# Kernel optimization log

Hardware: AMD Instinct MI355X
Metric: run time of the kernel (lower is better)

## Reference

```python
import jax, jax.numpy as jnp
import numpy as np

T_DIM, BATCH, D_DATA, H_HID = 128, 512, 512, 512
EPS = 1e-8  # torch cosine_similarity eps


def setup_inputs() -> dict:
    key = jax.random.key(0)
    k1, k2, k3, k4, k5 = jax.random.split(key, 5)
    s = 1.0 / np.sqrt(H_HID)  # torch LSTM default init scale
    return {
        "X_tilde": jax.random.normal(k1, (BATCH, T_DIM, D_DATA), jnp.float32),
        "W_ih": jax.random.normal(k2, (4 * H_HID, D_DATA), jnp.float32) * s,
        "W_hh": jax.random.normal(k3, (4 * H_HID, H_HID), jnp.float32) * s,
        "b_ih": jax.random.normal(k4, (4 * H_HID,), jnp.float32) * s,
        "b_hh": jax.random.normal(k5, (4 * H_HID,), jnp.float32) * s,
    }


def _ta_forward(X_tilde, W_ih, W_hh, b_ih, b_hh):
    B, T, D = X_tilde.shape
    H = W_hh.shape[1]

    def lstm_step(carry, x_t):  # x_t: [B, D]
        h, c = carry
        gates = x_t @ W_ih.T + h @ W_hh.T + (b_ih + b_hh)  # [B, 4H]
        i, f, g, o = jnp.split(gates, 4, axis=-1)  # torch gate order i,f,g,o
        i, f, o = jax.nn.sigmoid(i), jax.nn.sigmoid(f), jax.nn.sigmoid(o)
        g = jnp.tanh(g)
        c = f * c + i * g
        h = o * jnp.tanh(c)
        return (h, c), h

    h0 = jnp.zeros((B, H), X_tilde.dtype)
    c0 = jnp.zeros((B, H), X_tilde.dtype)
    # only the first T-1 inputs are fed to the LSTM (last hidden stored pre-step)
    xs = jnp.swapaxes(X_tilde[:, : T - 1, :], 0, 1)  # [T-1, B, D]
    _, hs = jax.lax.scan(lstm_step, (h0, c0), xs)  # [T-1, B, H]
    hidden_tensor = jnp.concatenate([h0[None], hs], axis=0)  # [T, B, H]

    # cosine similarity of each prior hidden (flattened over batch*H) vs final hidden
    ht_prior = hidden_tensor[:-1].reshape(T - 1, -1)  # [T-1, B*H]
    ht_fin = hidden_tensor[-1].reshape(-1)  # [B*H]
    num = ht_prior @ ht_fin  # [T-1]
    denom = jnp.maximum(jnp.linalg.norm(ht_prior, axis=1), EPS) * \
            jnp.maximum(jnp.linalg.norm(ht_fin), EPS)
    alpha = jax.nn.softmax(num / denom, axis=0)  # [T-1]

    ht_final = jnp.sum(alpha[:, None, None] * hidden_tensor[:-1], axis=0)  # [B, H]
    return ht_final[None]  # [1, B, H]


def reference(X_tilde, W_ih, W_hh, b_ih, b_hh):
    return _ta_forward(X_tilde, W_ih, W_hh, b_ih, b_hh)
```

## Files before the change

kernel.cpp:

```cpp
#include <hip/hip_runtime.h>
#include <stdint.h>

#define T_DIM  128
#define TSTEPS 127
#define BATCH  512
#define DDATA  512
#define HHID   512
#define BH     262144
#define CPAD   132

typedef _Float16 f16;
typedef _Float16 f16x8 __attribute__((ext_vector_type(8)));
typedef float    f32x4 __attribute__((ext_vector_type(4)));
typedef unsigned int u32x2 __attribute__((ext_vector_type(2)));

#define MFMA16 __builtin_amdgcn_mfma_f32_16x16x32_f16

__device__ __forceinline__ f16x8 ld16(const f16* p) {
  f16x8 r;
  asm volatile("global_load_dwordx4 %0, %1, off" : "=v"(r) : "v"(p));
  return r;
}
__device__ __forceinline__ f16x8 ld16cc(const f16* p) {
  f16x8 r;
  asm volatile("global_load_dwordx4 %0, %1, off sc0 sc1" : "=v"(r) : "v"(p));
  return r;
}
__device__ __forceinline__ void st8cc(void* p, u32x2 v) {
  asm volatile("global_store_dwordx2 %0, %1, off sc0 sc1" :: "v"(p), "v"(v) : "memory");
}

#define BAR_LGKM do { asm volatile("s_waitcnt lgkmcnt(0)\n\ts_barrier" ::: "memory"); } while (0)

__global__ void k_prep_w(const float* __restrict__ W_ih, const float* __restrict__ W_hh,
                         f16* __restrict__ W16B) {
  int d = blockIdx.x * blockDim.x + threadIdx.x;
  int lane = d & 63;
  int fi   = (d >> 6) & 31;
  int ch   = (d >> 11) & 1;
  int kq   = (d >> 12) & 3;
  int nbv  = d >> 14;
  int ks = fi >> 2, nf = fi & 3;
  int col16 = lane & 15, lk2 = lane >> 4;
  int hm = col16 >> 2, g = col16 & 3;
  int hg = nbv * 32 + (ch * 4 + nf) * 4 + hm;
  int R = g * 512 + hg;
  int k = kq * 256 + ks * 32 + lk2 * 8;
  const float* src = (k < 512) ? (W_ih + (size_t)R * 512 + k)
                               : (W_hh + (size_t)R * 512 + (k - 512));
  f16x8 o;
#pragma unroll
  for (int e = 0; e < 8; e++) o[e] = (f16)src[e];
  *(f16x8*)(W16B + (size_t)d * 8) = o;
}

__global__ void k_prep_b(const float* __restrict__ b_ih, const float* __restrict__ b_hh,
                         float* __restrict__ biasR) {
  int r = blockIdx.x * blockDim.x + threadIdx.x;
  if (r < 2048) biasR[r] = b_ih[r] + b_hh[r];
}

__global__ void k_prep_x(const float* __restrict__ X, f16* __restrict__ XT) {
  __shared__ f16 Ls[32][516];
  const int t = blockIdx.x;
  const int rb = blockIdx.y;
  const int tid = threadIdx.x;
  const int rloc = tid >> 5;
  const int dc = (tid & 31) * 16;
#pragma unroll
  for (int it = 0; it < 4; it++) {
    int row = it * 8 + rloc;
    const float* src = X + (size_t)(rb * 32 + row) * (T_DIM * DDATA)
                         + (size_t)t * DDATA + dc;
    f32x4 a0 = *(const f32x4*)(src);
    f32x4 a1 = *(const f32x4*)(src + 4);
    f32x4 a2 = *(const f32x4*)(src + 8);
    f32x4 a3 = *(const f32x4*)(src + 12);
    f16x8 h0, h1;
#pragma unroll
    for (int e = 0; e < 4; e++) {
      h0[e] = (f16)a0[e]; h0[4 + e] = (f16)a1[e];
      h1[e] = (f16)a2[e]; h1[4 + e] = (f16)a3[e];
    }
    *(f16x8*)&Ls[row][dc] = h0;
    *(f16x8*)&Ls[row][dc + 8] = h1;
  }
  __syncthreads();
#pragma unroll
  for (int it = 0; it < 8; it++) {
    int chunk = it * 256 + tid;
    int kc = chunk >> 5, row = chunk & 31;
    f16x8 v = *(const f16x8*)&Ls[row][kc * 8];
    *(f16x8*)(XT + (size_t)t * BH + (size_t)kc * 4096
              + (size_t)(rb * 32 + row) * 8) = v;
  }
}

__launch_bounds__(512, 1)
__global__ void k_lstm(const f16* __restrict__ XT, f16* __restrict__ h_all,
                       const f16* __restrict__ W16B, const float* __restrict__ biasR) {
  __shared__ float C[4][32][CPAD];
  __shared__ float BiasS[128];

  const int tid = threadIdx.x, lane = tid & 63, w = tid >> 6;
  const int kq = w >> 1;
  const int wg = blockIdx.x;
  const int mb = (wg & 7) * 2 + ((wg >> 3) & 1);
  const int nb = wg >> 4;
  const int m0 = mb * 32;
  const int l15 = lane & 15, lk = lane >> 4;

  f16x8 B[32];
  {
    const f16* wb = W16B + ((size_t)((nb * 4 + kq) * 2 + (w & 1)) * 32) * 512 + lane * 8;
#pragma unroll
    for (int i = 0; i < 32; i++) B[i] = ld16(wb + i * 512);
    asm volatile("s_waitcnt vmcnt(0)" ::: "memory");
    __builtin_amdgcn_sched_barrier(0);
  }
  if (tid < 128) {
    int q8 = tid >> 4, hm = (tid >> 2) & 3, g = tid & 3;
    BiasS[tid] = biasR[g * 512 + nb * 32 + q8 * 4 + hm];
  }
  float c_reg[4] = {0.f, 0.f, 0.f, 0.f};
  __syncthreads();

#define WAITV(N) asm volatile("s_waitcnt vmcnt(" #N ")" ::: "memory");        \
                 __builtin_amdgcn_sched_barrier(0)
#define MFMA4KS(KS0)                                                          \
    {                                                                         \
      _Pragma("unroll")                                                       \
      for (int s = 0; s < 4; s++) {                                           \
        int ks = KS0 + s;                                                     \
        _Pragma("unroll")                                                     \
        for (int nf = 0; nf < 4; nf++) {                                      \
          acc[0][nf] = MFMA16(R[2 * ks],     B[ks * 4 + nf], acc[0][nf], 0, 0, 0); \
          acc[1][nf] = MFMA16(R[2 * ks + 1], B[ks * 4 + nf], acc[1][nf], 0, 0, 0); \
        }                                                                     \
      }                                                                       \
    }
#define ISSUE_X(T)                                                            \
    {                                                                         \
      const f16* Ab = XT + (size_t)(T) * BH + (size_t)(kq * 32 + lk) * 4096   \
                      + (size_t)(m0 + l15) * 8;                               \
      _Pragma("unroll")                                                       \
      for (int ks = 0; ks < 8; ks++) {                                        \
        R[2 * ks]     = ld16(Ab + (size_t)ks * 16384);                        \
        R[2 * ks + 1] = ld16(Ab + (size_t)ks * 16384 + 128);                  \
      }                                                                       \
    }

  f16x8 R[16];
  if (kq < 2) ISSUE_X(0);

  for (int t = 0; t < TSTEPS; t++) {
    f32x4 acc[2][4] = {};

    if (kq < 2) {
      WAITV(0);
      MFMA4KS(0);
      MFMA4KS(4);
      if (t + 1 < TSTEPS) ISSUE_X(t + 1);
    } else if (t > 0) {
      const f16* Hb = h_all + (size_t)t * BH + (size_t)((kq - 2) * 32 + lk) * 4096
                      + (size_t)(m0 + l15) * 8;
      int rounds = 0;
      while (true) {
#pragma unroll
        for (int ks = 0; ks < 8; ks++) {
          R[2 * ks]     = ld16cc(Hb + (size_t)ks * 16384);
          R[2 * ks + 1] = ld16cc(Hb + (size_t)ks * 16384 + 128);
        }
        WAITV(0);
        unsigned bad = 0;
#pragma unroll
        for (int i = 0; i < 16; i++) {
          const unsigned* u = (const unsigned*)&R[i];
          bad |= (unsigned)(u[0] == 0xFFFFFFFFu) | (unsigned)(u[2] == 0xFFFFFFFFu);
        }
        if (__all(bad == 0)) break;
        if (++rounds > 4096) break;
        __builtin_amdgcn_s_sleep(1);
      }
      MFMA4KS(0);
      MFMA4KS(4);
    }

#pragma unroll
    for (int mf = 0; mf < 2; mf++)
#pragma unroll
      for (int nf = 0; nf < 4; nf++)
#pragma unroll
        for (int r = 0; r < 4; r++)
          C[kq][mf * 16 + lk * 4 + r][(w & 1) * 64 + nf * 16 + l15] = acc[mf][nf][r];
    BAR_LGKM;

    if (tid < 256) {
      int r = tid >> 3, q8 = tid & 7;
      f32x4 uu[4] = {};
#pragma unroll
      for (int q = 0; q < 4; q++) {
        const f32x4* base = (const f32x4*)&C[q][r][q8 * 16];
        uu[0] += base[0];
        uu[1] += base[1];
        uu[2] += base[2];
        uu[3] += base[3];
      }
      union { f16 h[4]; u32x2 v; } pk;
#pragma unroll
      for (int hm = 0; hm < 4; hm++) {
        float gi = uu[hm][0] + BiasS[q8 * 16 + hm * 4 + 0];
        float gf = uu[hm][1] + BiasS[q8 * 16 + hm * 4 + 1];
        float gg = uu[hm][2] + BiasS[q8 * 16 + hm * 4 + 2];
        float go = uu[hm][3] + BiasS[q8 * 16 + hm * 4 + 3];
        float ii = 1.f / (1.f + __expf(-gi));
        float ff = 1.f / (1.f + __expf(-gf));
        float eg = __expf(-2.f * fabsf(gg));
        float tg = copysignf((1.f - eg) / (1.f + eg), gg);
        float oo = 1.f / (1.f + __expf(-go));
        c_reg[hm] = ff * c_reg[hm] + ii * tg;
        float ec = __expf(-2.f * fabsf(c_reg[hm]));
        float th = copysignf((1.f - ec) / (1.f + ec), c_reg[hm]);
        pk.h[hm] = (f16)(oo * th);
      }
      f16* dst = h_all + (size_t)(t + 1) * BH
                 + (size_t)(nb * 4 + (q8 >> 1)) * 4096 + (size_t)(m0 + r) * 8
                 + (q8 & 1) * 4;
      st8cc(dst, pk.v);
    }
    BAR_LGKM;
  }
#undef WAITV
#undef MFMA4KS
#undef ISSUE_X
}

__global__ void k_dots(const f16* __restrict__ h_all, float* __restrict__ part) {
  int t = blockIdx.x, s = blockIdx.y;
  const f16x8* ht = (const f16x8*)(h_all + (size_t)t * BH) + (size_t)s * 8192;
  const f16x8* hf = (const f16x8*)(h_all + (size_t)127 * BH) + (size_t)s * 8192;
  float sn = 0.f, sq = 0.f;
  for (int i = threadIdx.x; i < 8192; i += 256) {
    f16x8 a = ht[i], b = hf[i];
#pragma unroll
    for (int e = 0; e < 8; e++) {
      float fa = (float)a[e], fb = (float)b[e];
      sn += fa * fb; sq += fa * fa;
    }
  }
  for (int off = 32; off; off >>= 1) {
    sn += __shfl_down(sn, off);
    sq += __shfl_down(sq, off);
  }
  __shared__ float red[8];
  int wid = threadIdx.x >> 6;
  if ((threadIdx.x & 63) == 0) { red[wid] = sn; red[4 + wid] = sq; }
  __syncthreads();
  if (threadIdx.x == 0) {
    part[t * 8 + s]     = red[0] + red[1] + red[2] + red[3];
    part[t * 8 + 4 + s] = red[4] + red[5] + red[6] + red[7];
  }
}

__global__ void k_softmax(float* __restrict__ part) {
  __shared__ float sn_s[128], sq_s[128];
  int t = threadIdx.x;
  if (t < 128) {
    float sn = part[t * 8 + 0] + part[t * 8 + 1] + part[t * 8 + 2] + part[t * 8 + 3];
    float sq = part[t * 8 + 4] + part[t * 8 + 5] + part[t * 8 + 6] + part[t * 8 + 7];
    sn_s[t] = sn; sq_s[t] = sq;
  }
  __syncthreads();
  if (t == 0) {
    float nf = fmaxf(sqrtf(sq_s[127]), 1e-8f);
    float m = -1e30f;
    for (int i = 0; i < TSTEPS; i++) {
      float np = fmaxf(sqrtf(sq_s[i]), 1e-8f);
      sn_s[i] = sn_s[i] / (np * nf);
      m = fmaxf(m, sn_s[i]);
    }
    float ssum = 0.f;
    for (int i = 0; i < TSTEPS; i++) { float e = __expf(sn_s[i] - m); sn_s[i] = e; ssum += e; }
    float inv = 1.f / ssum;
    for (int i = 0; i < TSTEPS; i++) part[1024 + i] = sn_s[i] * inv;
  }
}

__global__ void k_out(const f16* __restrict__ h_all, const float* __restrict__ part,
                      float* __restrict__ out) {
  __shared__ float al[TSTEPS];
  if (threadIdx.x < TSTEPS) al[threadIdx.x] = part[1024 + threadIdx.x];
  __syncthreads();
  int g = blockIdx.x * blockDim.x + threadIdx.x;
  int kc = g >> 9, row = g & 511;
  float s[8] = {0.f, 0.f, 0.f, 0.f, 0.f, 0.f, 0.f, 0.f};
  for (int t = 1; t < TSTEPS; t++) {
    f16x8 v = *(const f16x8*)(h_all + (size_t)t * BH + (size_t)kc * 4096 + row * 8);
    float a = al[t];
#pragma unroll
    for (int e = 0; e < 8; e++) s[e] += a * (float)v[e];
  }
  float* o = out + (size_t)row * 512 + kc * 8;
  f32x4 lo = {s[0], s[1], s[2], s[3]}, hi = {s[4], s[5], s[6], s[7]};
  *(f32x4*)o = lo;
  *(f32x4*)(o + 4) = hi;
}

extern "C" void kernel_launch(void* const* d_in, const int* in_sizes, int n_in,
                              void* d_out, int out_size, void* d_ws, size_t ws_size,
                              hipStream_t stream) {
  const float* X    = (const float*)d_in[0];
  const float* W_ih = (const float*)d_in[1];
  const float* W_hh = (const float*)d_in[2];
  const float* b_ih = (const float*)d_in[3];
  const float* b_hh = (const float*)d_in[4];

  char* ws = (char*)d_ws;
  size_t off = 0;
  auto alloc = [&](size_t bytes) -> void* {
    void* p = ws + off;
    off = (off + bytes + 255) & ~(size_t)255;
    return p;
  };
  f16*   W16B  = (f16*)  alloc((size_t)2048 * 1024 * 2);
  float* biasR = (float*)alloc(2048 * 4);
  f16*   XT    = (f16*)  alloc((size_t)TSTEPS * BH * 2);
  f16*   h_all = (f16*)  alloc((size_t)T_DIM * BH * 2);
  float* part  = (float*)alloc(2048 * 4);

  hipMemsetAsync(h_all, 0, (size_t)BH * 2, stream);
  hipMemsetAsync(h_all + BH, 0xFF, (size_t)TSTEPS * BH * 2, stream);

  k_prep_w<<<1024, 256, 0, stream>>>(W_ih, W_hh, W16B);
  k_prep_b<<<8, 256, 0, stream>>>(b_ih, b_hh, biasR);
  k_prep_x<<<dim3(TSTEPS, 16), 256, 0, stream>>>(X, XT);

  k_lstm<<<256, 512, 0, stream>>>(XT, h_all, W16B, biasR);

  k_dots<<<dim3(128, 4), 256, 0, stream>>>(h_all, part);
  k_softmax<<<1, 128, 0, stream>>>(part);
  k_out<<<128, 256, 0, stream>>>(h_all, part, (float*)d_out);
}
```

Measured before the change: 631.8 us.

## Replace sentinel polling with per-step atomic counters for cross-block LSTM sync

```diff
diff --git a/kernel.cpp b/kernel.cpp
--- a/kernel.cpp
+++ b/kernel.cpp
@@ -12,7 +12,6 @@
 typedef _Float16 f16;
 typedef _Float16 f16x8 __attribute__((ext_vector_type(8)));
 typedef float    f32x4 __attribute__((ext_vector_type(4)));
-typedef unsigned int u32x2 __attribute__((ext_vector_type(2)));
 
 #define MFMA16 __builtin_amdgcn_mfma_f32_16x16x32_f16
 
@@ -26,11 +25,6 @@
   asm volatile("global_load_dwordx4 %0, %1, off sc0 sc1" : "=v"(r) : "v"(p));
   return r;
 }
-__device__ __forceinline__ void st8cc(void* p, u32x2 v) {
-  asm volatile("global_store_dwordx2 %0, %1, off sc0 sc1" :: "v"(p), "v"(v) : "memory");
-}
-
-#define BAR_LGKM do { asm volatile("s_waitcnt lgkmcnt(0)\n\ts_barrier" ::: "memory"); } while (0)
 
 __global__ void k_prep_w(const float* __restrict__ W_ih, const float* __restrict__ W_hh,
                          f16* __restrict__ W16B) {
@@ -98,9 +92,10 @@
 
 __launch_bounds__(512, 1)
 __global__ void k_lstm(const f16* __restrict__ XT, f16* __restrict__ h_all,
-                       const f16* __restrict__ W16B, const float* __restrict__ biasR) {
+                       const f16* __restrict__ W16B, const float* __restrict__ biasR,
+                       int* __restrict__ done) {
   __shared__ float C[4][32][CPAD];
-  __shared__ float BiasS[128];
+  __shared__ int goS;
 
   const int tid = threadIdx.x, lane = tid & 63, w = tid >> 6;
   const int kq = w >> 1;
@@ -118,11 +113,16 @@
     asm volatile("s_waitcnt vmcnt(0)" ::: "memory");
     __builtin_amdgcn_sched_barrier(0);
   }
-  if (tid < 128) {
-    int q8 = tid >> 4, hm = (tid >> 2) & 3, g = tid & 3;
-    BiasS[tid] = biasR[g * 512 + nb * 32 + q8 * 4 + hm];
-  }
-  float c_reg[4] = {0.f, 0.f, 0.f, 0.f};
+  const int rloc = tid >> 4, hp = tid & 15;
+  const int hg0 = nb * 32 + 2 * hp;
+  float bv[8];
+#pragma unroll
+  for (int e = 0; e < 8; e++)
+    bv[e] = biasR[(e & 3) * 512 + nb * 32 + 2 * hp + (e >> 2)];
+  float c0 = 0.f, c1 = 0.f;
+  unsigned int* hdst_base = (unsigned int*)(h_all
+      + (size_t)(hg0 >> 3) * 4096 + (size_t)(m0 + rloc) * 8 + (hg0 & 7));
+  if (tid == 0) goS = 0;
   __syncthreads();
 
 #define WAITV(N) asm volatile("s_waitcnt vmcnt(" #N ")" ::: "memory");        \
@@ -162,28 +162,32 @@
       MFMA4KS(4);
       if (t + 1 < TSTEPS) ISSUE_X(t + 1);
     } else if (t > 0) {
+      if (w == 4) {
+        if (lane == 0) {
+          const int* flag = done + (size_t)(mb * 128 + (t - 1)) * 16;
+          int spins = 0;
+          while (__hip_atomic_load(flag, __ATOMIC_RELAXED, __HIP_MEMORY_SCOPE_AGENT) < 16) {
+            __builtin_amdgcn_s_sleep(1);
+            if (++spins > (1 << 20)) break;
+          }
+          __hip_atomic_store(&goS, t, __ATOMIC_RELAXED, __HIP_MEMORY_SCOPE_WORKGROUP);
+        }
+      } else {
+        int spins = 0;
+        while (__hip_atomic_load(&goS, __ATOMIC_RELAXED, __HIP_MEMORY_SCOPE_WORKGROUP) < t) {
+          __builtin_amdgcn_s_sleep(1);
+          if (++spins > (1 << 20)) break;
+        }
+      }
       const f16* Hb = h_all + (size_t)t * BH + (size_t)((kq - 2) * 32 + lk) * 4096
                       + (size_t)(m0 + l15) * 8;
-      int rounds = 0;
-      while (true) {
-#pragma unroll
-        for (int ks = 0; ks < 8; ks++) {
-          R[2 * ks]     = ld16cc(Hb + (size_t)ks * 16384);
-          R[2 * ks + 1] = ld16cc(Hb + (size_t)ks * 16384 + 128);
-        }
-        WAITV(0);
-        unsigned bad = 0;
-#pragma unroll
-        for (int i = 0; i < 16; i++) {
-          const unsigned* u = (const unsigned*)&R[i];
-          bad |= (unsigned)(u[0] == 0xFFFFFFFFu) | (unsigned)(u[2] == 0xFFFFFFFFu);
-        }
-        if (__all(bad == 0)) break;
-        if (++rounds > 4096) break;
-        __builtin_amdgcn_s_sleep(1);
+#pragma unroll
+      for (int ks = 0; ks < 8; ks++) {
+        R[2 * ks]     = ld16cc(Hb + (size_t)ks * 16384);
+        R[2 * ks + 1] = ld16cc(Hb + (size_t)ks * 16384 + 128);
       }
-      MFMA4KS(0);
-      MFMA4KS(4);
+      WAITV(8);  MFMA4KS(0);
+      WAITV(0);  MFMA4KS(4);
     }
 
 #pragma unroll
@@ -193,42 +197,54 @@
 #pragma unroll
         for (int r = 0; r < 4; r++)
           C[kq][mf * 16 + lk * 4 + r][(w & 1) * 64 + nf * 16 + l15] = acc[mf][nf][r];
-    BAR_LGKM;
-
-    if (tid < 256) {
-      int r = tid >> 3, q8 = tid & 7;
-      f32x4 uu[4] = {};
+    __syncthreads();
+
+    {
+      f32x4 u0 = {0.f, 0.f, 0.f, 0.f}, u1 = {0.f, 0.f, 0.f, 0.f};
 #pragma unroll
       for (int q = 0; q < 4; q++) {
-        const f32x4* base = (const f32x4*)&C[q][r][q8 * 16];
-        uu[0] += base[0];
-        uu[1] += base[1];
-        uu[2] += base[2];
-        uu[3] += base[3];
+        u0 += *(const f32x4*)&C[q][rloc][hp * 8];
+        u1 += *(const f32x4*)&C[q][rloc][hp * 8 + 4];
       }
-      union { f16 h[4]; u32x2 v; } pk;
-#pragma unroll
-      for (int hm = 0; hm < 4; hm++) {
-        float gi = uu[hm][0] + BiasS[q8 * 16 + hm * 4 + 0];
-        float gf = uu[hm][1] + BiasS[q8 * 16 + hm * 4 + 1];
-        float gg = uu[hm][2] + BiasS[q8 * 16 + hm * 4 + 2];
-        float go = uu[hm][3] + BiasS[q8 * 16 + hm * 4 + 3];
-        float ii = 1.f / (1.f + __expf(-gi));
-        float ff = 1.f / (1.f + __expf(-gf));
-        float eg = __expf(-2.f * fabsf(gg));
-        float tg = copysignf((1.f - eg) / (1.f + eg), gg);
-        float oo = 1.f / (1.f + __expf(-go));
-        c_reg[hm] = ff * c_reg[hm] + ii * tg;
-        float ec = __expf(-2.f * fabsf(c_reg[hm]));
-        float th = copysignf((1.f - ec) / (1.f + ec), c_reg[hm]);
-        pk.h[hm] = (f16)(oo * th);
-      }
-      f16* dst = h_all + (size_t)(t + 1) * BH
-                 + (size_t)(nb * 4 + (q8 >> 1)) * 4096 + (size_t)(m0 + r) * 8
-                 + (q8 & 1) * 4;
-      st8cc(dst, pk.v);
-    }
-    BAR_LGKM;
+      float gi0 = u0[0] + bv[0];
+      float gf0 = u0[1] + bv[1];
+      float gg0 = u0[2] + bv[2];
+      float go0 = u0[3] + bv[3];
+      float gi1 = u1[0] + bv[4];
+      float gf1 = u1[1] + bv[5];
+      float gg1 = u1[2] + bv[6];
+      float go1 = u1[3] + bv[7];
+
+      float i0 = 1.f / (1.f + __expf(-gi0));
+      float f0 = 1.f / (1.f + __expf(-gf0));
+      float e0 = __expf(-2.f * fabsf(gg0));
+      float tg0 = copysignf((1.f - e0) / (1.f + e0), gg0);
+      float o0 = 1.f / (1.f + __expf(-go0));
+      c0 = f0 * c0 + i0 * tg0;
+      float ec0 = __expf(-2.f * fabsf(c0));
+      float th0 = copysignf((1.f - ec0) / (1.f + ec0), c0);
+      float h0 = o0 * th0;
+
+      float i1 = 1.f / (1.f + __expf(-gi1));
+      float f1 = 1.f / (1.f + __expf(-gf1));
+      float e1 = __expf(-2.f * fabsf(gg1));
+      float tg1 = copysignf((1.f - e1) / (1.f + e1), gg1);
+      float o1 = 1.f / (1.f + __expf(-go1));
+      c1 = f1 * c1 + i1 * tg1;
+      float ec1 = __expf(-2.f * fabsf(c1));
+      float th1 = copysignf((1.f - ec1) / (1.f + ec1), c1);
+      float h1 = o1 * th1;
+
+      union { f16 h[2]; unsigned int u; } pk;
+      pk.h[0] = (f16)h0; pk.h[1] = (f16)h1;
+      __hip_atomic_store(hdst_base + (size_t)(t + 1) * (BH / 2), pk.u,
+                         __ATOMIC_RELAXED, __HIP_MEMORY_SCOPE_AGENT);
+    }
+    asm volatile("s_waitcnt vmcnt(0)" ::: "memory");
+    __syncthreads();
+    if (tid == 0)
+      __hip_atomic_fetch_add(done + (size_t)(mb * 128 + t) * 16, 1,
+                             __ATOMIC_RELAXED, __HIP_MEMORY_SCOPE_AGENT);
   }
 #undef WAITV
 #undef MFMA4KS
@@ -326,16 +342,17 @@
   float* biasR = (float*)alloc(2048 * 4);
   f16*   XT    = (f16*)  alloc((size_t)TSTEPS * BH * 2);
   f16*   h_all = (f16*)  alloc((size_t)T_DIM * BH * 2);
+  int*   done  = (int*)  alloc(16 * 128 * 64);
   float* part  = (float*)alloc(2048 * 4);
 
   hipMemsetAsync(h_all, 0, (size_t)BH * 2, stream);
-  hipMemsetAsync(h_all + BH, 0xFF, (size_t)TSTEPS * BH * 2, stream);
+  hipMemsetAsync(done,  0, 16 * 128 * 64, stream);
 
   k_prep_w<<<1024, 256, 0, stream>>>(W_ih, W_hh, W16B);
   k_prep_b<<<8, 256, 0, stream>>>(b_ih, b_hh, biasR);
   k_prep_x<<<dim3(TSTEPS, 16), 256, 0, stream>>>(X, XT);
 
-  k_lstm<<<256, 512, 0, stream>>>(XT, h_all, W16B, biasR);
+  k_lstm<<<256, 512, 0, stream>>>(XT, h_all, W16B, biasR, done);
 
   k_dots<<<dim3(128, 4), 256, 0, stream>>>(h_all, part);
   k_softmax<<<1, 128, 0, stream>>>(part);
```

Result: faster. 571.9 us (median of 2 runs) (-9.5%).

## Replace sentinel-polling of hidden states with per-row-block counter flags

Applied to the files above, without the earlier changes.

```diff
diff --git a/kernel.cpp b/kernel.cpp
--- a/kernel.cpp
+++ b/kernel.cpp
@@ -29,8 +29,6 @@
 __device__ __forceinline__ void st8cc(void* p, u32x2 v) {
   asm volatile("global_store_dwordx2 %0, %1, off sc0 sc1" :: "v"(p), "v"(v) : "memory");
 }
-
-#define BAR_LGKM do { asm volatile("s_waitcnt lgkmcnt(0)\n\ts_barrier" ::: "memory"); } while (0)
 
 __global__ void k_prep_w(const float* __restrict__ W_ih, const float* __restrict__ W_hh,
                          f16* __restrict__ W16B) {
@@ -98,9 +96,12 @@
 
 __launch_bounds__(512, 1)
 __global__ void k_lstm(const f16* __restrict__ XT, f16* __restrict__ h_all,
-                       const f16* __restrict__ W16B, const float* __restrict__ biasR) {
-  __shared__ float C[4][32][CPAD];
+                       const f16* __restrict__ W16B, const float* __restrict__ biasR,
+                       int* __restrict__ done) {
+  __shared__ float C[2][4][32][CPAD];
   __shared__ float BiasS[128];
+  __shared__ int goS;
+  __shared__ int cntS;
 
   const int tid = threadIdx.x, lane = tid & 63, w = tid >> 6;
   const int kq = w >> 1;
@@ -122,8 +123,11 @@
     int q8 = tid >> 4, hm = (tid >> 2) & 3, g = tid & 3;
     BiasS[tid] = biasR[g * 512 + nb * 32 + q8 * 4 + hm];
   }
+  if (tid == 0) { goS = 0; cntS = 0; }
   float c_reg[4] = {0.f, 0.f, 0.f, 0.f};
   __syncthreads();
+
+  int* flagline = done + (size_t)(mb * 128) * 16;
 
 #define WAITV(N) asm volatile("s_waitcnt vmcnt(" #N ")" ::: "memory");        \
                  __builtin_amdgcn_sched_barrier(0)
@@ -155,6 +159,7 @@
 
   for (int t = 0; t < TSTEPS; t++) {
     f32x4 acc[2][4] = {};
+    float (*Cb)[32][CPAD] = C[t & 1];
 
     if (kq < 2) {
       WAITV(0);
@@ -162,28 +167,32 @@
       MFMA4KS(4);
       if (t + 1 < TSTEPS) ISSUE_X(t + 1);
     } else if (t > 0) {
+      if (w == 4) {
+        if (lane == 0) {
+          const int* flag = flagline + (size_t)(t - 1) * 16;
+          int spins = 0;
+          while (__hip_atomic_load(flag, __ATOMIC_RELAXED, __HIP_MEMORY_SCOPE_AGENT) < 16) {
+            __builtin_amdgcn_s_sleep(1);
+            if (++spins > (1 << 14)) break;
+          }
+          __hip_atomic_store(&goS, t, __ATOMIC_RELAXED, __HIP_MEMORY_SCOPE_WORKGROUP);
+        }
+      } else {
+        int spins = 0;
+        while (__hip_atomic_load(&goS, __ATOMIC_RELAXED, __HIP_MEMORY_SCOPE_WORKGROUP) < t) {
+          __builtin_amdgcn_s_sleep(1);
+          if (++spins > (1 << 16)) break;
+        }
+      }
       const f16* Hb = h_all + (size_t)t * BH + (size_t)((kq - 2) * 32 + lk) * 4096
                       + (size_t)(m0 + l15) * 8;
-      int rounds = 0;
-      while (true) {
-#pragma unroll
-        for (int ks = 0; ks < 8; ks++) {
-          R[2 * ks]     = ld16cc(Hb + (size_t)ks * 16384);
-          R[2 * ks + 1] = ld16cc(Hb + (size_t)ks * 16384 + 128);
-        }
-        WAITV(0);
-        unsigned bad = 0;
-#pragma unroll
-        for (int i = 0; i < 16; i++) {
-          const unsigned* u = (const unsigned*)&R[i];
-          bad |= (unsigned)(u[0] == 0xFFFFFFFFu) | (unsigned)(u[2] == 0xFFFFFFFFu);
-        }
-        if (__all(bad == 0)) break;
-        if (++rounds > 4096) break;
-        __builtin_amdgcn_s_sleep(1);
-      }
-      MFMA4KS(0);
-      MFMA4KS(4);
+#pragma unroll
+      for (int ks = 0; ks < 8; ks++) {
+        R[2 * ks]     = ld16cc(Hb + (size_t)ks * 16384);
+        R[2 * ks + 1] = ld16cc(Hb + (size_t)ks * 16384 + 128);
+      }
+      WAITV(8);  MFMA4KS(0);
+      WAITV(0);  MFMA4KS(4);
     }
 
 #pragma unroll
@@ -192,15 +201,15 @@
       for (int nf = 0; nf < 4; nf++)
 #pragma unroll
         for (int r = 0; r < 4; r++)
-          C[kq][mf * 16 + lk * 4 + r][(w & 1) * 64 + nf * 16 + l15] = acc[mf][nf][r];
-    BAR_LGKM;
-
-    if (tid < 256) {
+          Cb[kq][mf * 16 + lk * 4 + r][(w & 1) * 64 + nf * 16 + l15] = acc[mf][nf][r];
+    __syncthreads();
+
+    if (kq < 2) {
       int r = tid >> 3, q8 = tid & 7;
       f32x4 uu[4] = {};
 #pragma unroll
       for (int q = 0; q < 4; q++) {
-        const f32x4* base = (const f32x4*)&C[q][r][q8 * 16];
+        const f32x4* base = (const f32x4*)&Cb[q][r][q8 * 16];
         uu[0] += base[0];
         uu[1] += base[1];
         uu[2] += base[2];
@@ -227,8 +236,20 @@
                  + (size_t)(nb * 4 + (q8 >> 1)) * 4096 + (size_t)(m0 + r) * 8
                  + (q8 & 1) * 4;
       st8cc(dst, pk.v);
-    }
-    BAR_LGKM;
+      WAITV(0);
+      if (lane == 0)
+        __hip_atomic_fetch_add(&cntS, 1, __ATOMIC_RELAXED, __HIP_MEMORY_SCOPE_WORKGROUP);
+      if (w == 0 && lane == 0) {
+        int spins = 0;
+        while (__hip_atomic_load(&cntS, __ATOMIC_RELAXED, __HIP_MEMORY_SCOPE_WORKGROUP)
+               < 4 * (t + 1)) {
+          __builtin_amdgcn_s_sleep(1);
+          if (++spins > (1 << 16)) break;
+        }
+        __hip_atomic_fetch_add(flagline + (size_t)t * 16, 1,
+                               __ATOMIC_RELAXED, __HIP_MEMORY_SCOPE_AGENT);
+      }
+    }
   }
 #undef WAITV
 #undef MFMA4KS
@@ -326,16 +347,17 @@
   float* biasR = (float*)alloc(2048 * 4);
   f16*   XT    = (f16*)  alloc((size_t)TSTEPS * BH * 2);
   f16*   h_all = (f16*)  alloc((size_t)T_DIM * BH * 2);
+  int*   done  = (int*)  alloc(16 * 128 * 64);
   float* part  = (float*)alloc(2048 * 4);
 
   hipMemsetAsync(h_all, 0, (size_t)BH * 2, stream);
-  hipMemsetAsync(h_all + BH, 0xFF, (size_t)TSTEPS * BH * 2, stream);
+  hipMemsetAsync(done,  0, 16 * 128 * 64, stream);
 
   k_prep_w<<<1024, 256, 0, stream>>>(W_ih, W_hh, W16B);
   k_prep_b<<<8, 256, 0, stream>>>(b_ih, b_hh, biasR);
   k_prep_x<<<dim3(TSTEPS, 16), 256, 0, stream>>>(X, XT);
 
-  k_lstm<<<256, 512, 0, stream>>>(XT, h_all, W16B, biasR);
+  k_lstm<<<256, 512, 0, stream>>>(XT, h_all, W16B, biasR, done);
 
   k_dots<<<dim3(128, 4), 256, 0, stream>>>(h_all, part);
   k_softmax<<<1, 128, 0, stream>>>(part);
```

New measurement: 793.1 us. +25.5%, slower.
